# Kernel tuning notes

Hardware: AMD Instinct MI355X
Metric: run time of the kernel (lower is better)

Reference implementation:

```python
import jax, jax.numpy as jnp
from jax import lax
import numpy as np

IN_CH = 32
OUT_CH = IN_CH // 4  # 8
K = 3

def _branch(x6, axis, w, b, a):
    # x6: [B, C, U, V, H, W]. Fold `axis` into batch, run one batched conv3d
    # over the remaining three spatio-angular dims (kernel 3, pad 1 == SAME),
    # then PReLU and unfold. Mathematically identical to the per-slice loop.
    x = jnp.moveaxis(x6, axis, 1)              # [B, L, C, d1, d2, d3]
    B, L = x.shape[0], x.shape[1]
    xr = x.reshape((B * L,) + x.shape[2:])      # [B*L, C, d1, d2, d3]
    y = lax.conv_general_dilated(
        xr, w, window_strides=(1, 1, 1), padding='SAME',
        dimension_numbers=('NCDHW', 'OIDHW', 'NCDHW'))
    y = y + b[None, :, None, None, None]
    y = jnp.where(y >= 0, y, a * y)             # PReLU (single shared slope)
    y = y.reshape((B, L) + y.shape[1:])         # [B, L, O, d1, d2, d3]
    return jnp.moveaxis(y, 1, axis)             # [B, O, U, V, H, W]

def setup_inputs() -> dict:
    key = jax.random.key(0)
    ks = jax.random.split(key, 9)
    fan_in = IN_CH * K * K * K
    bound = 1.0 / np.sqrt(fan_in)
    x = jax.random.normal(ks[0], (8, IN_CH, 5, 5, 64, 64), dtype=jnp.float32)
    def mk_w(k):
        return jax.random.uniform(k, (OUT_CH, IN_CH, K, K, K), jnp.float32, -bound, bound)
    def mk_b(k):
        return jax.random.uniform(k, (OUT_CH,), jnp.float32, -bound, bound)
    inp = {'x': x}
    for i, name in enumerate(['uvx', 'uvy', 'uxy', 'vxy']):
        inp[f'w_{name}'] = mk_w(ks[1 + 2 * i])
        inp[f'b_{name}'] = mk_b(ks[2 + 2 * i])
        inp[f'a_{name}'] = jnp.full((1,), 0.25, dtype=jnp.float32)  # PReLU init
    return inp

def reference(x, w_uvx, b_uvx, a_uvx, w_uvy, b_uvy, a_uvy,
              w_uxy, b_uxy, a_uxy, w_vxy, b_vxy, a_vxy):
    # x: [B, C, U, V, H, W]
    uvx = _branch(x, 5, w_uvx, b_uvx, a_uvx)  # conv over (U, V, H), slice W
    uvy = _branch(x, 4, w_uvy, b_uvy, a_uvy)  # conv over (U, V, W), slice H
    uxy = _branch(x, 3, w_uxy, b_uxy, a_uxy)  # conv over (U, H, W), slice V
    vxy = _branch(x, 2, w_vxy, b_vxy, a_vxy)  # conv over (V, H, W), slice U
    return jnp.concatenate([uvx, uvy, uxy, vxy], axis=1)
```

## Files before the change

kernel.cpp:

```cpp
#include <hip/hip_runtime.h>

#define B_  8
#define C_  32
#define U_  5
#define V_  5
#define H_  64
#define W_  64

#define SV_ 4096
#define SU_ 20480
#define SC_ 102400
#define SB_ 3276800

#define XROW 4224
#define BT_OFF 54067200ull

typedef short bf16x8 __attribute__((ext_vector_type(8)));
typedef float f32x4 __attribute__((ext_vector_type(4)));

__device__ __forceinline__ unsigned short f2bf(float f) {
    unsigned int u = __builtin_bit_cast(unsigned int, f);
    u = (u + 0x7FFFu + ((u >> 16) & 1u)) >> 16;
    return (unsigned short)u;
}

__device__ __forceinline__ f32x4 mfma16(bf16x8 a, bf16x8 b, f32x4 c) {
    return __builtin_amdgcn_mfma_f32_16x16x32_bf16(a, b, c, 0, 0, 0);
}

__global__ __launch_bounds__(256)
void k_transpose(const float* __restrict__ x, unsigned short* __restrict__ xT)
{
    __shared__ float tl[C_ * 4 * 64];
    const int tid = threadIdx.x;
    int blk = blockIdx.x;
    const int hq = blk & 15; blk >>= 4;
    const int v = blk % 5; blk /= 5;
    const int u = blk % 5;
    const int b = blk / 5;
    const int h0 = hq * 4;

    const float* src = x + (size_t)b * SB_ + (size_t)u * SU_ + (size_t)v * SV_ + h0 * 64;
#pragma unroll
    for (int i = 0; i < 8; ++i) {
        const int e = tid + i * 256;
        const int c = e >> 6;
        const int rem = e & 63;
        const int h = rem >> 4;
        const int w4 = (rem & 15) * 4;
        const float4 val = *(const float4*)(src + (size_t)c * SC_ + h * 64 + w4);
        *(float4*)(tl + c * 256 + h * 64 + w4) = val;
    }
    __syncthreads();

    const int h = tid >> 6;
    const int w = tid & 63;
    unsigned short* dst = xT + (size_t)((b * 25 + u * 5 + v) * 64 + h0 + h) * (XROW / 2);
    const uint4 z = make_uint4(0u, 0u, 0u, 0u);
#pragma unroll
    for (int cq = 0; cq < 4; ++cq) {
        unsigned short s[8];
#pragma unroll
        for (int j = 0; j < 8; ++j)
            s[j] = f2bf(tl[(cq * 8 + j) * 256 + h * 64 + w]);
        uint4 o;
        o.x = (unsigned)s[0] | ((unsigned)s[1] << 16);
        o.y = (unsigned)s[2] | ((unsigned)s[3] << 16);
        o.z = (unsigned)s[4] | ((unsigned)s[5] << 16);
        o.w = (unsigned)s[6] | ((unsigned)s[7] << 16);
        *(uint4*)(dst + cq * 528 + (w + 1) * 8) = o;
        if (w == 0)  *(uint4*)(dst + cq * 528 + 0)       = z;
        if (w == 63) *(uint4*)(dst + cq * 528 + 65 * 8)  = z;
    }
}

__global__ __launch_bounds__(256)
void k_weights(const float* __restrict__ w0, const float* __restrict__ w1,
               const float* __restrict__ w2, const float* __restrict__ w3,
               unsigned short* __restrict__ btab)
{
    const int f = blockIdx.x;
    const int br = f / 27;
    const int tap = f % 27;
    const float* wp = (br == 0) ? w0 : (br == 1) ? w1 : (br == 2) ? w2 : w3;
    const int q  = threadIdx.x >> 6;
    const int oc = (threadIdx.x >> 3) & 7;
    const int j  = threadIdx.x & 7;
    btab[(size_t)f * 256 + q * 64 + oc * 8 + j] =
        f2bf(wp[(size_t)oc * 864 + (q * 8 + j) * 27 + tap]);
}

__global__ __launch_bounds__(512, 2)
void k_main(const unsigned short* __restrict__ xT,
            const unsigned short* __restrict__ btabu,
            const float* __restrict__ bb0, const float* __restrict__ aa0,
            const float* __restrict__ bb1, const float* __restrict__ aa1,
            const float* __restrict__ bb2, const float* __restrict__ aa2,
            const float* __restrict__ bb3, const float* __restrict__ aa3,
            float* __restrict__ out)
{
    __shared__ alignas(16) char wlds[55296];

    const int tid = threadIdx.x;
    const int blk = blockIdx.x;
    const int buv = (blk & 7) + 8 * (blk >> 7);
    const int hs  = (blk >> 3) & 15;
    const int v = buv % 5;
    const int u = (buv / 5) % 5;
    const int b = buv / 25;
    const int h0 = hs * 4;

    {
        const uint4* g = (const uint4*)btabu;
        uint4* l = (uint4*)wlds;
#pragma unroll
        for (int i = 0; i < 7; ++i) {
            const int e = tid + i * 512;
            if (e < 3456) l[e] = g[e];
        }
    }
    __syncthreads();

    const int wave = tid >> 6;
    const int lane = tid & 63;
    const int n = lane & 15;
    const int q = lane >> 4;
    const int w0 = (wave & 3) * 16;
    const int rbase = (wave >> 2) * 2;

    f32x4 acc[4][2];
#pragma unroll
    for (int i = 0; i < 4; ++i)
#pragma unroll
        for (int j = 0; j < 2; ++j) acc[i][j] = (f32x4)0.f;

    const char* xTb = (const char*)xT;
    const int lane_off = q * 1056 + (w0 + n) * 16;

    auto WF = [&](int f) -> bf16x8 {
        return *(const bf16x8*)(wlds + f * 512 + q * 128 + (n & 7) * 16);
    };
    const bf16x8 zf = {0, 0, 0, 0, 0, 0, 0, 0};

#pragma unroll
    for (int du = 0; du < 3; ++du) {
        const int up = u + du - 1;
        if (up < 0 || up >= 5) continue;
#pragma unroll
        for (int dv = 0; dv < 3; ++dv) {
            const int vp = v + dv - 1;
            if (vp < 0 || vp >= 5) continue;

            const size_t rowb = (size_t)((b * 25 + up * 5 + vp) * 64) * XROW;
            bf16x8 F[4][3];
#pragma unroll
            for (int r = 0; r < 4; ++r) {
                const int hr = h0 + rbase + r - 1;
                if (hr < 0 || hr >= 64) {
                    F[r][0] = zf; F[r][1] = zf; F[r][2] = zf;
                } else {
                    const char* p = xTb + rowb + (size_t)hr * XROW + lane_off;
#pragma unroll
                    for (int dw = 0; dw < 3; ++dw)
                        F[r][dw] = *(const bf16x8*)(p + dw * 16);
                }
            }

#pragma unroll
            for (int t = 0; t < 3; ++t) {
                const bf16x8 Wf = WF(du * 9 + dv * 3 + t);
                acc[0][0] = mfma16(Wf, F[t + 0][1], acc[0][0]);
                acc[0][1] = mfma16(Wf, F[t + 1][1], acc[0][1]);
            }
#pragma unroll
            for (int dw = 0; dw < 3; ++dw) {
                const bf16x8 Wf = WF(27 + du * 9 + dv * 3 + dw);
                acc[1][0] = mfma16(Wf, F[1][dw], acc[1][0]);
                acc[1][1] = mfma16(Wf, F[2][dw], acc[1][1]);
            }
            if (dv == 1) {
#pragma unroll
                for (int dh = 0; dh < 3; ++dh)
#pragma unroll
                    for (int dw = 0; dw < 3; ++dw) {
                        const bf16x8 Wf = WF(54 + du * 9 + dh * 3 + dw);
                        acc[2][0] = mfma16(Wf, F[dh + 0][dw], acc[2][0]);
                        acc[2][1] = mfma16(Wf, F[dh + 1][dw], acc[2][1]);
                    }
            }
            if (du == 1) {
#pragma unroll
                for (int dh = 0; dh < 3; ++dh)
#pragma unroll
                    for (int dw = 0; dw < 3; ++dw) {
                        const bf16x8 Wf = WF(81 + dv * 9 + dh * 3 + dw);
                        acc[3][0] = mfma16(Wf, F[dh + 0][dw], acc[3][0]);
                        acc[3][1] = mfma16(Wf, F[dh + 1][dw], acc[3][1]);
                    }
            }
        }
    }

    const float alph[4] = { aa0[0], aa1[0], aa2[0], aa3[0] };
    float* op = out + (size_t)b * SB_ + (size_t)u * SU_ + (size_t)v * SV_ + w0 + n;
    const bool act = (q < 2);
#pragma unroll
    for (int br = 0; br < 4; ++br) {
        const float* bp = (br == 0) ? bb0 : (br == 1) ? bb1 : (br == 2) ? bb2 : bb3;
        const f32x4 bv = *(const f32x4*)(bp + (q & 1) * 4);
#pragma unroll
        for (int hh = 0; hh < 2; ++hh) {
            const int h = h0 + rbase + hh;
#pragma unroll
            for (int r = 0; r < 4; ++r) {
                float val = acc[br][hh][r] + bv[r];
                val = (val >= 0.f) ? val : alph[br] * val;
                if (act)
                    op[(size_t)(br * 8 + q * 4 + r) * SC_ + (size_t)h * 64] = val;
            }
        }
    }
}

extern "C" void kernel_launch(void* const* d_in, const int* in_sizes, int n_in,
                              void* d_out, int out_size, void* d_ws, size_t ws_size,
                              hipStream_t stream) {
    const float* x  = (const float*)d_in[0];
    const float* w0 = (const float*)d_in[1];
    const float* b0 = (const float*)d_in[2];
    const float* a0 = (const float*)d_in[3];
    const float* w1 = (const float*)d_in[4];
    const float* b1 = (const float*)d_in[5];
    const float* a1 = (const float*)d_in[6];
    const float* w2 = (const float*)d_in[7];
    const float* b2 = (const float*)d_in[8];
    const float* a2 = (const float*)d_in[9];
    const float* w3 = (const float*)d_in[10];
    const float* b3 = (const float*)d_in[11];
    const float* a3 = (const float*)d_in[12];
    float* out = (float*)d_out;

    unsigned short* xT = (unsigned short*)d_ws;
    unsigned short* bt = (unsigned short*)((char*)d_ws + BT_OFF);

    k_weights<<<108, 256, 0, stream>>>(w0, w1, w2, w3, bt);
    k_transpose<<<B_ * U_ * V_ * (H_ / 4), 256, 0, stream>>>(x, xT);
    k_main<<<B_ * U_ * V_ * (H_ / 4), 512, 0, stream>>>(
        xT, bt, b0, a0, b1, a1, b2, a2, b3, a3, out);
}
```

Before: 297.1 us.

## Merge prep kernels and give each wave four output rows to reuse loaded rows

The weight-conversion kernel is folded into the transpose kernel as extra blocks, which removes one launch. The main kernel now has each wave compute four H rows instead of two. It loads six input rows per dw shift and reuses them across more MFMAs, and the grid is halved to 1600 blocks. Block ordering changes so that consecutive blocks differ in batch. The trade-off is more accumulator registers (16 f32x4) and fewer blocks, which may lower occupancy or leave CUs under-filled.

```diff
diff --git a/kernel.cpp b/kernel.cpp
--- a/kernel.cpp
+++ b/kernel.cpp
@@ -29,8 +29,24 @@
 }
 
 __global__ __launch_bounds__(256)
-void k_transpose(const float* __restrict__ x, unsigned short* __restrict__ xT)
+void k_prep(const float* __restrict__ x, unsigned short* __restrict__ xT,
+            const float* __restrict__ w0, const float* __restrict__ w1,
+            const float* __restrict__ w2, const float* __restrict__ w3,
+            unsigned short* __restrict__ btab)
 {
+    if (blockIdx.x >= 3200) {
+        const int f = blockIdx.x - 3200;
+        const int br = f / 27;
+        const int tap = f % 27;
+        const float* wp = (br == 0) ? w0 : (br == 1) ? w1 : (br == 2) ? w2 : w3;
+        const int q  = threadIdx.x >> 6;
+        const int oc = (threadIdx.x >> 3) & 7;
+        const int j  = threadIdx.x & 7;
+        btab[(size_t)f * 256 + q * 64 + oc * 8 + j] =
+            f2bf(wp[(size_t)oc * 864 + (q * 8 + j) * 27 + tap]);
+        return;
+    }
+
     __shared__ float tl[C_ * 4 * 64];
     const int tid = threadIdx.x;
     int blk = blockIdx.x;
@@ -74,22 +90,6 @@
     }
 }
 
-__global__ __launch_bounds__(256)
-void k_weights(const float* __restrict__ w0, const float* __restrict__ w1,
-               const float* __restrict__ w2, const float* __restrict__ w3,
-               unsigned short* __restrict__ btab)
-{
-    const int f = blockIdx.x;
-    const int br = f / 27;
-    const int tap = f % 27;
-    const float* wp = (br == 0) ? w0 : (br == 1) ? w1 : (br == 2) ? w2 : w3;
-    const int q  = threadIdx.x >> 6;
-    const int oc = (threadIdx.x >> 3) & 7;
-    const int j  = threadIdx.x & 7;
-    btab[(size_t)f * 256 + q * 64 + oc * 8 + j] =
-        f2bf(wp[(size_t)oc * 864 + (q * 8 + j) * 27 + tap]);
-}
-
 __global__ __launch_bounds__(512, 2)
 void k_main(const unsigned short* __restrict__ xT,
             const unsigned short* __restrict__ btabu,
@@ -103,19 +103,20 @@
 
     const int tid = threadIdx.x;
     const int blk = blockIdx.x;
-    const int buv = (blk & 7) + 8 * (blk >> 7);
-    const int hs  = (blk >> 3) & 15;
+    const int b   = blk & 7;
+    const int i   = blk >> 3;
+    const int buv = i >> 3;
+    const int hs  = i & 7;
     const int v = buv % 5;
-    const int u = (buv / 5) % 5;
-    const int b = buv / 25;
-    const int h0 = hs * 4;
+    const int u = buv / 5;
+    const int h0 = hs * 8;
 
     {
         const uint4* g = (const uint4*)btabu;
         uint4* l = (uint4*)wlds;
 #pragma unroll
-        for (int i = 0; i < 7; ++i) {
-            const int e = tid + i * 512;
+        for (int it = 0; it < 7; ++it) {
+            const int e = tid + it * 512;
             if (e < 3456) l[e] = g[e];
         }
     }
@@ -126,13 +127,14 @@
     const int n = lane & 15;
     const int q = lane >> 4;
     const int w0 = (wave & 3) * 16;
-    const int rbase = (wave >> 2) * 2;
-
-    f32x4 acc[4][2];
-#pragma unroll
-    for (int i = 0; i < 4; ++i)
-#pragma unroll
-        for (int j = 0; j < 2; ++j) acc[i][j] = (f32x4)0.f;
+    const int rbase = (wave >> 2) * 4;
+    const int hb = h0 + rbase;
+
+    f32x4 acc[4][4];
+#pragma unroll
+    for (int a = 0; a < 4; ++a)
+#pragma unroll
+        for (int j = 0; j < 4; ++j) acc[a][j] = (f32x4)0.f;
 
     const char* xTb = (const char*)xT;
     const int lane_off = q * 1056 + (w0 + n) * 16;
@@ -151,52 +153,51 @@
             const int vp = v + dv - 1;
             if (vp < 0 || vp >= 5) continue;
 
-            const size_t rowb = (size_t)((b * 25 + up * 5 + vp) * 64) * XROW;
-            bf16x8 F[4][3];
-#pragma unroll
-            for (int r = 0; r < 4; ++r) {
-                const int hr = h0 + rbase + r - 1;
-                if (hr < 0 || hr >= 64) {
-                    F[r][0] = zf; F[r][1] = zf; F[r][2] = zf;
-                } else {
-                    const char* p = xTb + rowb + (size_t)hr * XROW + lane_off;
-#pragma unroll
-                    for (int dw = 0; dw < 3; ++dw)
-                        F[r][dw] = *(const bf16x8*)(p + dw * 16);
-                }
-            }
-
-#pragma unroll
-            for (int t = 0; t < 3; ++t) {
-                const bf16x8 Wf = WF(du * 9 + dv * 3 + t);
-                acc[0][0] = mfma16(Wf, F[t + 0][1], acc[0][0]);
-                acc[0][1] = mfma16(Wf, F[t + 1][1], acc[0][1]);
-            }
+            const char* base = xTb + (size_t)((b * 25 + up * 5 + vp) * 64) * XROW + lane_off;
+
 #pragma unroll
             for (int dw = 0; dw < 3; ++dw) {
-                const bf16x8 Wf = WF(27 + du * 9 + dv * 3 + dw);
-                acc[1][0] = mfma16(Wf, F[1][dw], acc[1][0]);
-                acc[1][1] = mfma16(Wf, F[2][dw], acc[1][1]);
-            }
-            if (dv == 1) {
-#pragma unroll
-                for (int dh = 0; dh < 3; ++dh)
-#pragma unroll
-                    for (int dw = 0; dw < 3; ++dw) {
+                bf16x8 F[6];
+#pragma unroll
+                for (int r = 0; r < 6; ++r) {
+                    const int hr = hb + r - 1;
+                    F[r] = (hr < 0 || hr >= 64) ? zf
+                         : *(const bf16x8*)(base + (size_t)hr * XROW + dw * 16);
+                }
+
+                if (dw == 1) {
+#pragma unroll
+                    for (int t = 0; t < 3; ++t) {
+                        const bf16x8 Wf = WF(du * 9 + dv * 3 + t);
+#pragma unroll
+                        for (int hh = 0; hh < 4; ++hh)
+                            acc[0][hh] = mfma16(Wf, F[t + hh], acc[0][hh]);
+                    }
+                }
+                {
+                    const bf16x8 Wf = WF(27 + du * 9 + dv * 3 + dw);
+#pragma unroll
+                    for (int hh = 0; hh < 4; ++hh)
+                        acc[1][hh] = mfma16(Wf, F[hh + 1], acc[1][hh]);
+                }
+                if (dv == 1) {
+#pragma unroll
+                    for (int dh = 0; dh < 3; ++dh) {
                         const bf16x8 Wf = WF(54 + du * 9 + dh * 3 + dw);
-                        acc[2][0] = mfma16(Wf, F[dh + 0][dw], acc[2][0]);
-                        acc[2][1] = mfma16(Wf, F[dh + 1][dw], acc[2][1]);
+#pragma unroll
+                        for (int hh = 0; hh < 4; ++hh)
+                            acc[2][hh] = mfma16(Wf, F[dh + hh], acc[2][hh]);
                     }
-            }
-            if (du == 1) {
-#pragma unroll
-                for (int dh = 0; dh < 3; ++dh)
-#pragma unroll
-                    for (int dw = 0; dw < 3; ++dw) {
+                }
+                if (du == 1) {
+#pragma unroll
+                    for (int dh = 0; dh < 3; ++dh) {
                         const bf16x8 Wf = WF(81 + dv * 9 + dh * 3 + dw);
-                        acc[3][0] = mfma16(Wf, F[dh + 0][dw], acc[3][0]);
-                        acc[3][1] = mfma16(Wf, F[dh + 1][dw], acc[3][1]);
+#pragma unroll
+                        for (int hh = 0; hh < 4; ++hh)
+                            acc[3][hh] = mfma16(Wf, F[dh + hh], acc[3][hh]);
                     }
+                }
             }
         }
     }
@@ -209,8 +210,8 @@
         const float* bp = (br == 0) ? bb0 : (br == 1) ? bb1 : (br == 2) ? bb2 : bb3;
         const f32x4 bv = *(const f32x4*)(bp + (q & 1) * 4);
 #pragma unroll
-        for (int hh = 0; hh < 2; ++hh) {
-            const int h = h0 + rbase + hh;
+        for (int hh = 0; hh < 4; ++hh) {
+            const int h = hb + hh;
 #pragma unroll
             for (int r = 0; r < 4; ++r) {
                 float val = acc[br][hh][r] + bv[r];
@@ -243,8 +244,7 @@
     unsigned short* xT = (unsigned short*)d_ws;
     unsigned short* bt = (unsigned short*)((char*)d_ws + BT_OFF);
 
-    k_weights<<<108, 256, 0, stream>>>(w0, w1, w2, w3, bt);
-    k_transpose<<<B_ * U_ * V_ * (H_ / 4), 256, 0, stream>>>(x, xT);
-    k_main<<<B_ * U_ * V_ * (H_ / 4), 512, 0, stream>>>(
+    k_prep<<<3200 + 108, 256, 0, stream>>>(x, xT, w0, w1, w2, w3, bt);
+    k_main<<<1600, 512, 0, stream>>>(
         xT, bt, b0, a0, b1, a1, b2, a2, b3, a3, out);
 }
```

After: 284.7 us. -4.2%, faster.
